# Kernel tuning notes

Hardware: AMD Instinct MI355X
Metric: run time of the kernel (lower is better)

## Reference

```python
import jax, jax.numpy as jnp
import numpy as np

D, H = 8, 1024        # data_dim, hidden_size
ENC, HOR = 96, 336    # encode window, prediction horizon


def _cell(x, h, c, wih, whh, b):
    # PyTorch LSTM gate order: i, f, g, o
    g = x @ wih.T + h @ whh.T + b
    i, f, gg, o = jnp.split(g, 4, axis=-1)
    c2 = jax.nn.sigmoid(f) * c + jax.nn.sigmoid(i) * jnp.tanh(gg)
    h2 = jax.nn.sigmoid(o) * jnp.tanh(c2)
    return h2, c2


def _run_layer(xs, wih, whh, b, h0, c0):
    # xs: [T, B, in] -> outputs [T, B, out], final (h, c)
    def step(carry, xt):
        h, c = carry
        h2, c2 = _cell(xt, h, c, wih, whh, b)
        return (h2, c2), h2
    (hT, cT), hs = jax.lax.scan(step, (h0, c0), xs)
    return hs, hT, cT


def setup_inputs() -> dict:
    key = jax.random.key(0)
    ks = jax.random.split(key, 10)
    s = 1.0 / np.sqrt(H)
    inputs = jax.random.normal(ks[0], (64, ENC + HOR, D), dtype=jnp.float32)
    # lstm (2 layers, hidden H)
    w_ih0 = jax.random.normal(ks[1], (4 * H, D), dtype=jnp.float32) * s
    w_hh0 = jax.random.normal(ks[2], (4 * H, H), dtype=jnp.float32) * s
    b0 = jax.random.normal(ks[3], (4 * H,), dtype=jnp.float32) * s
    w_ih1 = jax.random.normal(ks[4], (4 * H, H), dtype=jnp.float32) * s
    w_hh1 = jax.random.normal(ks[5], (4 * H, H), dtype=jnp.float32) * s
    b1 = jax.random.normal(ks[6], (4 * H,), dtype=jnp.float32) * s
    # lstm2 (1 layer, hidden D)
    w_ih2 = jax.random.normal(ks[7], (4 * D, H), dtype=jnp.float32) * s
    w_hh2 = jax.random.normal(ks[8], (4 * D, D), dtype=jnp.float32) * s
    b2 = jax.random.normal(ks[9], (4 * D,), dtype=jnp.float32) * s
    return {"inputs": inputs, "w_ih0": w_ih0, "w_hh0": w_hh0, "b0": b0,
            "w_ih1": w_ih1, "w_hh1": w_hh1, "b1": b1,
            "w_ih2": w_ih2, "w_hh2": w_hh2, "b2": b2}


def reference(inputs, w_ih0, w_hh0, b0, w_ih1, w_hh1, b1, w_ih2, w_hh2, b2):
    x = inputs[..., :D]
    enc, y = x[:, :ENC], x[:, ENC:]          # [B,96,D], [B,336,D]
    B = enc.shape[0]
    zH = jnp.zeros((B, H), dtype=enc.dtype)
    zD = jnp.zeros((B, D), dtype=enc.dtype)

    # ---- encode: stacked LSTM over 96 steps ----
    xs = enc.transpose(1, 0, 2)              # [T,B,D]
    h1s, ha, ca = _run_layer(xs, w_ih0, w_hh0, b0, zH, zH)
    h2s, hb, cb = _run_layer(h1s, w_ih1, w_hh1, b1, zH, zH)
    hds, hd, cd = _run_layer(h2s, w_ih2, w_hh2, b2, zD, zD)
    pred0 = hds[-1]                          # [B,D]

    def dec(carry, _):
        p, ha, ca, hb, cb, hd, cd = carry
        ha, ca = _cell(p, ha, ca, w_ih0, w_hh0, b0)
        hb, cb = _cell(ha, hb, cb, w_ih1, w_hh1, b1)
        hd, cd = _cell(hb, hd, cd, w_ih2, w_hh2, b2)
        return (hd, ha, ca, hb, cb, hd, cd), hd

    _, preds = jax.lax.scan(dec, (pred0, ha, ca, hb, cb, hd, cd), None,
                            length=HOR - 1)  # [335,B,D]
    pred = jnp.concatenate([pred0[None], preds], axis=0).transpose(1, 0, 2)  # [B,336,D]
    loss = jnp.mean((pred - y) ** 2, axis=(0, 1))  # [D]
    return pred, y, loss
```

## Files before the change

kernel.cpp:

```cpp
#include <hip/hip_runtime.h>
#include <math.h>

#define B64 64
#define H 1024
#define DD 8
#define ENC 96
#define HOR 336
#define TT 432
#define NSTEP 431
#define NBLK 256
#define KS0 32
#define KS1 64
#define RSEG 392
#define RCOL 24

typedef __attribute__((ext_vector_type(8))) short short8;
typedef __attribute__((ext_vector_type(4))) float f32x4;
typedef __attribute__((ext_vector_type(4))) unsigned int u32x4;
typedef unsigned long long ull;

__device__ __forceinline__ unsigned short f2bf(float x) {
    union { float f; unsigned u; } v; v.f = x;
    unsigned r = v.u + 0x7fffu + ((v.u >> 16) & 1u);
    return (unsigned short)(r >> 16);
}
__device__ __forceinline__ float sigm(float x) {
    return __builtin_amdgcn_rcpf(1.0f + __expf(-x));
}
__device__ __forceinline__ float ftanh(float x) {
    float e = __expf(fminf(x, 10.0f) * 2.0f);
    return (e - 1.0f) * __builtin_amdgcn_rcpf(e + 1.0f);
}

__device__ __forceinline__ short8 cload16(const unsigned short* p) {
    u32x4 v;
    asm volatile("global_load_dwordx4 %0, %1, off sc0 sc1"
                 : "=v"(v) : "v"(p) : "memory");
    union { u32x4 u; short8 s; } c; c.u = v; return c.s;
}
__device__ __forceinline__ void cstore16(unsigned short* p, ull lo, ull hi) {
    union { ull u[2]; u32x4 v; } c; c.u[0] = lo; c.u[1] = hi;
    asm volatile("global_store_dwordx4 %0, %1, off sc0 sc1"
                 :: "v"(p), "v"(c.v) : "memory");
}
__device__ __forceinline__ void kwait() {
    asm volatile("s_waitcnt vmcnt(0)" ::: "memory");
    __builtin_amdgcn_sched_barrier(0);
}


__global__ void zero_k(unsigned int* __restrict__ p, int n) {
    for (int i = blockIdx.x * 256 + threadIdx.x; i < n; i += gridDim.x * 256) p[i] = 0u;
}

__global__ void pack0_k(const float* __restrict__ w, unsigned short* __restrict__ dst) {
    const int total = 128 * 2 * KS0 * 64 * 8;
    for (int idx = blockIdx.x * 256 + threadIdx.x; idx < total; idx += gridDim.x * 256) {
        int j = idx & 7, lane = (idx >> 3) & 63, ks = (idx >> 9) & 31, nt = (idx >> 14) & 1, nb = idx >> 15;
        int rr = nt * 16 + (lane & 15);
        int row = nb * 8 + (rr >> 2) + 1024 * (rr & 3);
        int k = ks * 32 + ((lane >> 4) << 3) + j;
        dst[idx] = f2bf(w[row * 1024 + k]);
    }
}

__global__ void pack1_k(const float* __restrict__ wih, const float* __restrict__ whh,
                        unsigned short* __restrict__ dst) {
    const int total = 128 * 2 * KS1 * 64 * 8;
    for (int idx = blockIdx.x * 256 + threadIdx.x; idx < total; idx += gridDim.x * 256) {
        int j = idx & 7, lane = (idx >> 3) & 63, ks = (idx >> 9) & 63, nt = (idx >> 15) & 1, nb = idx >> 16;
        int rr = nt * 16 + (lane & 15);
        int row = nb * 8 + (rr >> 2) + 1024 * (rr & 3);
        int k = ks * 32 + ((lane >> 4) << 3) + j;
        float v = (k < 1024) ? wih[row * 1024 + k] : whh[row * 1024 + (k - 1024)];
        dst[idx] = f2bf(v);
    }
}

__global__ void pack2_k(const float* __restrict__ w, unsigned short* __restrict__ dst) {
    const int total = 2 * KS0 * 64 * 8;
    for (int idx = blockIdx.x * 256 + threadIdx.x; idx < total; idx += gridDim.x * 256) {
        int j = idx & 7, lane = (idx >> 3) & 63, ks = (idx >> 9) & 31, nt = (idx >> 14) & 1;
        int rr = nt * 16 + (lane & 15);
        int row = (rr >> 2) + 8 * (rr & 3);
        int k = ks * 32 + ((lane >> 4) << 3) + j;
        dst[idx] = f2bf(w[row * 1024 + k]);
    }
}

__global__ void copy_y_k(const float* __restrict__ inp, float* __restrict__ y) {
    const int total = B64 * HOR * DD;
    for (int i = blockIdx.x * 256 + threadIdx.x; i < total; i += gridDim.x * 256) {
        int b = i / (HOR * DD);
        int rem = i - b * (HOR * DD);
        y[i] = inp[b * (TT * DD) + ENC * DD + rem];
    }
}

__global__ void loss_k(const float* __restrict__ pred, const float* __restrict__ y,
                       float* __restrict__ loss) {
    __shared__ float part[256];
    int tid = threadIdx.x;
    int dd = tid & 7, cc = tid >> 3;
    float s = 0.f;
    for (int i = cc; i < B64 * HOR; i += 32) {
        float d = pred[i * 8 + dd] - y[i * 8 + dd];
        s += d * d;
    }
    part[tid] = s;
    __syncthreads();
    if (tid < 8) {
        float t = 0.f;
        for (int r = 0; r < 32; ++r) t += part[r * 8 + tid];
        loss[tid] = t / (float)(B64 * HOR);
    }
}

__device__ __forceinline__ void gbar_arrive(unsigned* dom, int rb, unsigned ep) {
    if (threadIdx.x == 0) {
        __builtin_amdgcn_s_waitcnt(0x0f70);
        __hip_atomic_store(dom + rb * 32, ep, __ATOMIC_RELAXED,
                           __HIP_MEMORY_SCOPE_SYSTEM);
    }
}
__device__ __forceinline__ void gbar_wait(unsigned* dom, unsigned ep) {
    const int tid = threadIdx.x;
    if (tid < 64) {
        const unsigned* f0 = dom + tid * 32;
        const unsigned* f1 = dom + (tid + 64) * 32;
        for (;;) {
            unsigned a = __hip_atomic_load(f0, __ATOMIC_RELAXED, __HIP_MEMORY_SCOPE_SYSTEM);
            unsigned b = __hip_atomic_load(f1, __ATOMIC_RELAXED, __HIP_MEMORY_SCOPE_SYSTEM);
            if (__all((a >= ep) && (b >= ep))) break;
        }
    }
    __syncthreads();
}

__global__ __launch_bounds__(256, 1) void persist_k(
    const unsigned short* __restrict__ Wp0,
    const unsigned short* __restrict__ Wp1,
    const unsigned short* __restrict__ Wp2,
    const float* __restrict__ wih0, const float* __restrict__ b0v,
    const float* __restrict__ b1v,
    const float* __restrict__ whh2, const float* __restrict__ b2v,
    const float* __restrict__ inp,
    unsigned short* __restrict__ H0a, unsigned short* __restrict__ H0b,
    unsigned short* __restrict__ H1a, unsigned short* __restrict__ H1b,
    unsigned* __restrict__ bar0, float* __restrict__ pred)
{
    const int tid = threadIdx.x;
    const int wv = tid >> 6, lane = tid & 63;
    const int blk = blockIdx.x;
    const int bg = blk & 1, rb = blk >> 1;
    const int bl = tid & 31, u = tid >> 5;
    const int mtl = bl >> 4, m16 = bl & 15;
    unsigned* dom = bar0 + (bg << 13);

    __shared__ float red1[16 * RSEG];
    __shared__ float red2[16 * RSEG];
    __shared__ float h2x[32 * 9];
    __shared__ ull hstage[32][3];

    for (int i = tid; i < 32 * 9; i += 256) h2x[i] = 0.f;

    short8 Wr0[2][8], Wr1h0[2][8], Wr1h1[2][8];
    {
        const short8* p0 = (const short8*)Wp0;
        const short8* p1 = (const short8*)Wp1;
        #pragma unroll
        for (int ot = 0; ot < 2; ++ot)
            #pragma unroll
            for (int kk = 0; kk < 8; ++kk) {
                Wr0[ot][kk]   = p0[((rb * 2 + ot) * KS0 + 8 * wv + kk) * 64 + lane];
                Wr1h0[ot][kk] = p1[((rb * 2 + ot) * KS1 + 8 * wv + kk) * 64 + lane];
                Wr1h1[ot][kk] = p1[((rb * 2 + ot) * KS1 + 32 + 8 * wv + kk) * 64 + lane];
            }
    }
    float wih0r[4][8], whh2r[4][8], b0r[4], b1r[4], b2r[4];
    #pragma unroll
    for (int g = 0; g < 4; ++g) {
        int row = rb * 8 + u + 1024 * g;
        #pragma unroll
        for (int d = 0; d < 8; ++d) wih0r[g][d] = wih0[row * 8 + d];
        b0r[g] = b0v[row];
        b1r[g] = b1v[row];
        int row2 = u + 8 * g;
        #pragma unroll
        for (int d = 0; d < 8; ++d) whh2r[g][d] = whh2[row2 * 8 + d];
        b2r[g] = b2v[row2];
    }
    float c0r = 0.f, c1r = 0.f, c2r = 0.f;
    unsigned ep = 0;

    auto redWrite = [&](float* red, f32x4 (&acc)[2][2]) {
        #pragma unroll
        for (int m = 0; m < 2; ++m)
            #pragma unroll
            for (int ot = 0; ot < 2; ++ot) {
                int base = ((wv * 2 + m) * 2 + ot) * RSEG + (lane & 15) * RCOL + (lane >> 4) * 4;
                #pragma unroll
                for (int r = 0; r < 4; ++r) red[base + r] = acc[m][ot][r];
            }
    };
    auto redSum = [&](const float* red, int g) {
        int rr = u * 4 + g, ot = rr >> 4, rr16 = rr & 15;
        float s = 0.f;
        #pragma unroll
        for (int w2i = 0; w2i < 4; ++w2i)
            s += red[((w2i * 2 + mtl) * 2 + ot) * RSEG + rr16 * RCOL + m16];
        return s;
    };
    auto hPublish = [&](unsigned short* Hw) {
        __syncthreads();
        if (tid < 32) {
            int b = bg * 32 + tid;
            int chunk = ((b >> 4) * KS0 + (rb >> 2)) * 64 + ((b & 15) | ((rb & 3) << 4));
            cstore16((unsigned short*)((ull*)Hw + chunk * 2),
                     hstage[tid][0], hstage[tid][1]);
        }
    };

    __syncthreads();

    f32x4 acc[2][2];
    #pragma unroll
    for (int m = 0; m < 2; ++m)
        #pragma unroll
        for (int ot = 0; ot < 2; ++ot) acc[m][ot] = (f32x4){0.f, 0.f, 0.f, 0.f};

    {
        float xv[8];
        int b = bg * 32 + bl;
        #pragma unroll
        for (int d = 0; d < 8; ++d) xv[d] = inp[(b * TT + 0) * DD + d];
        float g4[4];
        #pragma unroll
        for (int g = 0; g < 4; ++g) {
            float s = b0r[g];
            #pragma unroll
            for (int d = 0; d < 8; ++d) s += wih0r[g][d] * xv[d];
            g4[g] = s;
        }
        c0r = sigm(g4[0]) * ftanh(g4[2]);
        float hn = sigm(g4[3]) * ftanh(c0r);
        ((unsigned short*)hstage)[bl * 12 + u] = f2bf(hn);
        hPublish(H0a);
    }
    gbar_arrive(dom, rb, ++ep);

    for (int t = 0; t < NSTEP; ++t) {
        const int par = t & 1;
        const unsigned short* H0cur = par ? H0b : H0a;
        unsigned short* H1w = par ? H1b : H1a;
        unsigned short* H0nxt = par ? H0a : H0b;
        const bool last = (t == NSTEP - 1);

        gbar_wait(dom, ep);

        short8 pa[8], pb[8];
        {
            #pragma unroll
            for (int kk = 0; kk < 8; ++kk) {
                pa[kk] = cload16(H0cur + (((bg * 2 + 0) * KS0 + 8 * wv + kk) * 64 + lane) * 8);
                pb[kk] = cload16(H0cur + (((bg * 2 + 1) * KS0 + 8 * wv + kk) * 64 + lane) * 8);
            }
            kwait();
            #pragma unroll
            for (int kk = 0; kk < 8; ++kk) {
                #pragma unroll
                for (int ot = 0; ot < 2; ++ot) {
                    acc[0][ot] = __builtin_amdgcn_mfma_f32_16x16x32_bf16(pa[kk], Wr1h0[ot][kk], acc[0][ot], 0, 0, 0);
                    acc[1][ot] = __builtin_amdgcn_mfma_f32_16x16x32_bf16(pb[kk], Wr1h0[ot][kk], acc[1][ot], 0, 0, 0);
                }
            }
            redWrite(red1, acc);
            __syncthreads();
            float g4[4];
            #pragma unroll
            for (int g = 0; g < 4; ++g) g4[g] = b1r[g] + redSum(red1, g);
            c1r = sigm(g4[1]) * c1r + sigm(g4[0]) * ftanh(g4[2]);
            float hn = sigm(g4[3]) * ftanh(c1r);
            ((unsigned short*)hstage)[bl * 12 + u] = f2bf(hn);
            hPublish(H1w);
        }

        if (!last) {
            f32x4 a1[2][2];
            #pragma unroll
            for (int m = 0; m < 2; ++m)
                #pragma unroll
                for (int ot = 0; ot < 2; ++ot) a1[m][ot] = (f32x4){0.f, 0.f, 0.f, 0.f};
            #pragma unroll
            for (int kk = 0; kk < 8; ++kk) {
                #pragma unroll
                for (int ot = 0; ot < 2; ++ot) {
                    a1[0][ot] = __builtin_amdgcn_mfma_f32_16x16x32_bf16(pa[kk], Wr0[ot][kk], a1[0][ot], 0, 0, 0);
                    a1[1][ot] = __builtin_amdgcn_mfma_f32_16x16x32_bf16(pb[kk], Wr0[ot][kk], a1[1][ot], 0, 0, 0);
                }
            }
            redWrite(red2, a1);
        }
        gbar_arrive(dom, rb, ++ep);
        gbar_wait(dom, ep);

        {
            const short8* p2w = (const short8*)Wp2;
            short8 w2[2][8];
            #pragma unroll
            for (int ot = 0; ot < 2; ++ot)
                #pragma unroll
                for (int kk = 0; kk < 8; ++kk)
                    w2[ot][kk] = p2w[(ot * KS0 + 8 * wv + kk) * 64 + lane];
            short8 qa[8], qb[8];
            #pragma unroll
            for (int kk = 0; kk < 8; ++kk) {
                qa[kk] = cload16(H1w + (((bg * 2 + 0) * KS0 + 8 * wv + kk) * 64 + lane) * 8);
                qb[kk] = cload16(H1w + (((bg * 2 + 1) * KS0 + 8 * wv + kk) * 64 + lane) * 8);
            }
            kwait();
            f32x4 a3[2][2];
            #pragma unroll
            for (int m = 0; m < 2; ++m)
                #pragma unroll
                for (int ot = 0; ot < 2; ++ot) a3[m][ot] = (f32x4){0.f, 0.f, 0.f, 0.f};
            #pragma unroll
            for (int kk = 0; kk < 8; ++kk) {
                #pragma unroll
                for (int ot = 0; ot < 2; ++ot) {
                    a3[0][ot] = __builtin_amdgcn_mfma_f32_16x16x32_bf16(qa[kk], w2[ot][kk], a3[0][ot], 0, 0, 0);
                    a3[1][ot] = __builtin_amdgcn_mfma_f32_16x16x32_bf16(qb[kk], w2[ot][kk], a3[1][ot], 0, 0, 0);
                }
            }
            redWrite(red1, a3);
            __syncthreads();
            float xo[8];
            #pragma unroll
            for (int d = 0; d < 8; ++d) xo[d] = h2x[bl * 9 + d];
            float g4[4];
            #pragma unroll
            for (int g = 0; g < 4; ++g) {
                float s = b2r[g] + redSum(red1, g);
                #pragma unroll
                for (int d = 0; d < 8; ++d) s += whh2r[g][d] * xo[d];
                g4[g] = s;
            }
            float cn = sigm(g4[1]) * c2r + sigm(g4[0]) * ftanh(g4[2]);
            c2r = cn;
            float hn2 = sigm(g4[3]) * ftanh(cn);
            __syncthreads();
            h2x[bl * 9 + u] = hn2;
            if (rb == 0 && t >= ENC - 1)
                pred[((bg * 32 + bl) * HOR + (t - (ENC - 1))) * DD + u] = hn2;

            if (!last) {
                __syncthreads();
                const int tt = t + 1;
                float xv[8];
                if (tt < ENC) {
                    int b = bg * 32 + bl;
                    #pragma unroll
                    for (int d = 0; d < 8; ++d) xv[d] = inp[(b * TT + tt) * DD + d];
                } else {
                    #pragma unroll
                    for (int d = 0; d < 8; ++d) xv[d] = h2x[bl * 9 + d];
                }
                float g1[4];
                #pragma unroll
                for (int g = 0; g < 4; ++g) {
                    float s = b0r[g] + redSum(red2, g);
                    #pragma unroll
                    for (int d = 0; d < 8; ++d) s += wih0r[g][d] * xv[d];
                    g1[g] = s;
                }
                c0r = sigm(g1[1]) * c0r + sigm(g1[0]) * ftanh(g1[2]);
                float hn0 = sigm(g1[3]) * ftanh(c0r);
                ((unsigned short*)hstage)[bl * 12 + u] = f2bf(hn0);
                hPublish(H0nxt);

                #pragma unroll
                for (int m = 0; m < 2; ++m)
                    #pragma unroll
                    for (int ot = 0; ot < 2; ++ot) acc[m][ot] = (f32x4){0.f, 0.f, 0.f, 0.f};
                #pragma unroll
                for (int kk = 0; kk < 8; ++kk) {
                    #pragma unroll
                    for (int ot = 0; ot < 2; ++ot) {
                        acc[0][ot] = __builtin_amdgcn_mfma_f32_16x16x32_bf16(qa[kk], Wr1h1[ot][kk], acc[0][ot], 0, 0, 0);
                        acc[1][ot] = __builtin_amdgcn_mfma_f32_16x16x32_bf16(qb[kk], Wr1h1[ot][kk], acc[1][ot], 0, 0, 0);
                    }
                }
                gbar_arrive(dom, rb, ++ep);
            }
        }
    }
}


extern "C" void kernel_launch(void* const* d_in, const int* in_sizes, int n_in,
                              void* d_out, int out_size, void* d_ws, size_t ws_size,
                              hipStream_t stream)
{
    const float* inp  = (const float*)d_in[0];
    const float* wih0 = (const float*)d_in[1];
    const float* whh0 = (const float*)d_in[2];
    const float* b0v  = (const float*)d_in[3];
    const float* wih1 = (const float*)d_in[4];
    const float* whh1 = (const float*)d_in[5];
    const float* b1v  = (const float*)d_in[6];
    const float* wih2 = (const float*)d_in[7];
    const float* whh2 = (const float*)d_in[8];
    const float* b2v  = (const float*)d_in[9];
    float* out = (float*)d_out;

    char* base = (char*)d_ws;
    size_t off = 0;
    auto carve = [&](size_t bytes) -> void* {
        void* p = base + off;
        off += (bytes + 255) & ~((size_t)255);
        return p;
    };
    unsigned short* Wp0 = (unsigned short*)carve((size_t)128 * 2 * KS0 * 64 * 8 * 2);
    unsigned short* Wp1 = (unsigned short*)carve((size_t)128 * 2 * KS1 * 64 * 8 * 2);
    unsigned short* Wp2 = (unsigned short*)carve((size_t)2 * KS0 * 64 * 8 * 2);
    size_t state_off = off;
    unsigned short* H0a = (unsigned short*)carve(B64 * H * 2);
    unsigned short* H0b = (unsigned short*)carve(B64 * H * 2);
    unsigned short* H1a = (unsigned short*)carve(B64 * H * 2);
    unsigned short* H1b = (unsigned short*)carve(B64 * H * 2);
    unsigned* bar = (unsigned*)carve(2 * 8192 * 4);
    size_t state_bytes = off - state_off;
    if (off > ws_size) return;

    zero_k<<<64, 256, 0, stream>>>((unsigned int*)(base + state_off), (int)(state_bytes / 4));
    pack0_k<<<2048, 256, 0, stream>>>(whh0, Wp0);
    pack1_k<<<4096, 256, 0, stream>>>(wih1, whh1, Wp1);
    pack2_k<<<32, 256, 0, stream>>>(wih2, Wp2);
    copy_y_k<<<672, 256, 0, stream>>>(inp, out + 172032);

    persist_k<<<NBLK, 256, 0, stream>>>(Wp0, Wp1, Wp2, wih0, b0v, b1v, whh2, b2v,
                                        inp, H0a, H0b, H1a, H1b, bar, out);

    loss_k<<<1, 256, 0, stream>>>(out, out + 172032, out + 344064);
}
```

Before: 3.483 ms.

## Fuse prep kernels into one launch, parallelize loss, and enlarge RSEG/RCOL

Merges the zeroing, three weight-packing kernels and the y copy into a single prep kernel, which removes four kernel launches and their gaps. The loss reduction now runs across 64 blocks and accumulates with atomicAdd into a loss buffer that the prep kernel zeroes. RSEG and RCOL are also increased, which changes how much work or shared space some part of the persistent kernel uses. Atomic accumulation makes the loss summation order nondeterministic.

```diff
diff --git a/kernel.cpp b/kernel.cpp
--- a/kernel.cpp
+++ b/kernel.cpp
@@ -11,8 +11,8 @@
 #define NBLK 256
 #define KS0 32
 #define KS1 64
-#define RSEG 392
-#define RCOL 24
+#define RSEG 440
+#define RCOL 28
 
 typedef __attribute__((ext_vector_type(8))) short short8;
 typedef __attribute__((ext_vector_type(4))) float f32x4;
@@ -49,51 +49,57 @@
 }
 
 
-__global__ void zero_k(unsigned int* __restrict__ p, int n) {
-    for (int i = blockIdx.x * 256 + threadIdx.x; i < n; i += gridDim.x * 256) p[i] = 0u;
-}
-
-__global__ void pack0_k(const float* __restrict__ w, unsigned short* __restrict__ dst) {
-    const int total = 128 * 2 * KS0 * 64 * 8;
-    for (int idx = blockIdx.x * 256 + threadIdx.x; idx < total; idx += gridDim.x * 256) {
-        int j = idx & 7, lane = (idx >> 3) & 63, ks = (idx >> 9) & 31, nt = (idx >> 14) & 1, nb = idx >> 15;
-        int rr = nt * 16 + (lane & 15);
-        int row = nb * 8 + (rr >> 2) + 1024 * (rr & 3);
-        int k = ks * 32 + ((lane >> 4) << 3) + j;
-        dst[idx] = f2bf(w[row * 1024 + k]);
-    }
-}
-
-__global__ void pack1_k(const float* __restrict__ wih, const float* __restrict__ whh,
-                        unsigned short* __restrict__ dst) {
-    const int total = 128 * 2 * KS1 * 64 * 8;
-    for (int idx = blockIdx.x * 256 + threadIdx.x; idx < total; idx += gridDim.x * 256) {
-        int j = idx & 7, lane = (idx >> 3) & 63, ks = (idx >> 9) & 63, nt = (idx >> 15) & 1, nb = idx >> 16;
-        int rr = nt * 16 + (lane & 15);
-        int row = nb * 8 + (rr >> 2) + 1024 * (rr & 3);
-        int k = ks * 32 + ((lane >> 4) << 3) + j;
-        float v = (k < 1024) ? wih[row * 1024 + k] : whh[row * 1024 + (k - 1024)];
-        dst[idx] = f2bf(v);
-    }
-}
-
-__global__ void pack2_k(const float* __restrict__ w, unsigned short* __restrict__ dst) {
-    const int total = 2 * KS0 * 64 * 8;
-    for (int idx = blockIdx.x * 256 + threadIdx.x; idx < total; idx += gridDim.x * 256) {
-        int j = idx & 7, lane = (idx >> 3) & 63, ks = (idx >> 9) & 31, nt = (idx >> 14) & 1;
-        int rr = nt * 16 + (lane & 15);
-        int row = (rr >> 2) + 8 * (rr & 3);
-        int k = ks * 32 + ((lane >> 4) << 3) + j;
-        dst[idx] = f2bf(w[row * 1024 + k]);
-    }
-}
-
-__global__ void copy_y_k(const float* __restrict__ inp, float* __restrict__ y) {
-    const int total = B64 * HOR * DD;
-    for (int i = blockIdx.x * 256 + threadIdx.x; i < total; i += gridDim.x * 256) {
-        int b = i / (HOR * DD);
-        int rem = i - b * (HOR * DD);
-        y[i] = inp[b * (TT * DD) + ENC * DD + rem];
+__global__ void prep_k(const float* __restrict__ whh0,
+                       const float* __restrict__ wih1, const float* __restrict__ whh1,
+                       const float* __restrict__ wih2, const float* __restrict__ inp,
+                       unsigned short* __restrict__ Wp0, unsigned short* __restrict__ Wp1,
+                       unsigned short* __restrict__ Wp2, float* __restrict__ y,
+                       unsigned int* __restrict__ zp, int zn, float* __restrict__ loss)
+{
+    const int stride = gridDim.x * 256;
+    const int base = blockIdx.x * 256 + threadIdx.x;
+
+    for (int i = base; i < zn; i += stride) zp[i] = 0u;
+    if (base < 8) loss[base] = 0.f;
+
+    {
+        const int total = 128 * 2 * KS0 * 64 * 8;
+        for (int idx = base; idx < total; idx += stride) {
+            int j = idx & 7, lane = (idx >> 3) & 63, ks = (idx >> 9) & 31, nt = (idx >> 14) & 1, nb = idx >> 15;
+            int rr = nt * 16 + (lane & 15);
+            int row = nb * 8 + (rr >> 2) + 1024 * (rr & 3);
+            int k = ks * 32 + ((lane >> 4) << 3) + j;
+            Wp0[idx] = f2bf(whh0[row * 1024 + k]);
+        }
+    }
+    {
+        const int total = 128 * 2 * KS1 * 64 * 8;
+        for (int idx = base; idx < total; idx += stride) {
+            int j = idx & 7, lane = (idx >> 3) & 63, ks = (idx >> 9) & 63, nt = (idx >> 15) & 1, nb = idx >> 16;
+            int rr = nt * 16 + (lane & 15);
+            int row = nb * 8 + (rr >> 2) + 1024 * (rr & 3);
+            int k = ks * 32 + ((lane >> 4) << 3) + j;
+            float v = (k < 1024) ? wih1[row * 1024 + k] : whh1[row * 1024 + (k - 1024)];
+            Wp1[idx] = f2bf(v);
+        }
+    }
+    {
+        const int total = 2 * KS0 * 64 * 8;
+        for (int idx = base; idx < total; idx += stride) {
+            int j = idx & 7, lane = (idx >> 3) & 63, ks = (idx >> 9) & 31, nt = (idx >> 14) & 1;
+            int rr = nt * 16 + (lane & 15);
+            int row = (rr >> 2) + 8 * (rr & 3);
+            int k = ks * 32 + ((lane >> 4) << 3) + j;
+            Wp2[idx] = f2bf(wih2[row * 1024 + k]);
+        }
+    }
+    {
+        const int total = B64 * HOR * DD;
+        for (int i = base; i < total; i += stride) {
+            int b = i / (HOR * DD);
+            int rem = i - b * (HOR * DD);
+            y[i] = inp[b * (TT * DD) + ENC * DD + rem];
+        }
     }
 }
 
@@ -103,7 +109,7 @@
     int tid = threadIdx.x;
     int dd = tid & 7, cc = tid >> 3;
     float s = 0.f;
-    for (int i = cc; i < B64 * HOR; i += 32) {
+    for (int i = blockIdx.x * 32 + cc; i < B64 * HOR; i += 64 * 32) {
         float d = pred[i * 8 + dd] - y[i * 8 + dd];
         s += d * d;
     }
@@ -112,7 +118,7 @@
     if (tid < 8) {
         float t = 0.f;
         for (int r = 0; r < 32; ++r) t += part[r * 8 + tid];
-        loss[tid] = t / (float)(B64 * HOR);
+        atomicAdd(&loss[tid], t * (1.0f / (float)(B64 * HOR)));
     }
 }
 
@@ -432,14 +438,13 @@
     size_t state_bytes = off - state_off;
     if (off > ws_size) return;
 
-    zero_k<<<64, 256, 0, stream>>>((unsigned int*)(base + state_off), (int)(state_bytes / 4));
-    pack0_k<<<2048, 256, 0, stream>>>(whh0, Wp0);
-    pack1_k<<<4096, 256, 0, stream>>>(wih1, whh1, Wp1);
-    pack2_k<<<32, 256, 0, stream>>>(wih2, Wp2);
-    copy_y_k<<<672, 256, 0, stream>>>(inp, out + 172032);
+    prep_k<<<2048, 256, 0, stream>>>(whh0, wih1, whh1, wih2, inp,
+                                     Wp0, Wp1, Wp2, out + 172032,
+                                     (unsigned int*)(base + state_off),
+                                     (int)(state_bytes / 4), out + 344064);
 
     persist_k<<<NBLK, 256, 0, stream>>>(Wp0, Wp1, Wp2, wih0, b0v, b1v, whh2, b2v,
                                         inp, H0a, H0b, H1a, H1b, bar, out);
 
-    loss_k<<<1, 256, 0, stream>>>(out, out + 172032, out + 344064);
-}
+    loss_k<<<64, 256, 0, stream>>>(out, out + 172032, out + 344064);
+}
```

Result: faster. 3.293 ms (-5.5%).
